# Optimization experiments

Hardware: AMD Instinct MI355X
Metric: run time of the kernel (lower is better)

## Reference

```python
import jax, jax.numpy as jnp
import numpy as np

B, N, S, K = 4, 32768, 8192, 16
IN_C, OUT_C = 64, 128
MID = max(OUT_C // 4, 8)  # attn_mlp hidden = 32
GN_GROUPS = 8
EPS = 1e-5


def setup_inputs() -> dict:
    key = jax.random.key(0)
    ks = jax.random.split(key, 16)
    def lin(k, out_c, in_c):
        # torch nn.Linear default init: U(-1/sqrt(in), 1/sqrt(in)), weight shape (out, in)
        bound = 1.0 / np.sqrt(in_c)
        return jax.random.uniform(k, (out_c, in_c), jnp.float32, -bound, bound)
    return {
        "xyz": jax.random.normal(ks[0], (B, N, 3), jnp.float32),
        "feats": jax.random.normal(ks[1], (B, N, IN_C), jnp.float32),
        "idx_fps": jax.random.randint(ks[2], (B, S), 0, N),
        "idx_knn": jax.random.randint(ks[3], (B, S, K), 0, N),
        "Wq": lin(ks[4], OUT_C, IN_C),
        "Wk": lin(ks[5], OUT_C, IN_C),
        "Wv": lin(ks[6], OUT_C, IN_C),
        "Wp1": lin(ks[7], OUT_C, 3),
        "Wp2": lin(ks[8], OUT_C, OUT_C),
        "Wa1": lin(ks[9], MID, OUT_C),
        "Wa2": lin(ks[10], OUT_C, MID),
        "Wproj": lin(ks[11], OUT_C, OUT_C),
        "ln_w": jnp.ones((OUT_C,), jnp.float32),
        "ln_b": jnp.zeros((OUT_C,), jnp.float32),
        "Wres": lin(ks[12], OUT_C, IN_C),
        "Wpost": lin(ks[13], OUT_C, OUT_C),
        "gn_w": jnp.ones((OUT_C,), jnp.float32),
        "gn_b": jnp.zeros((OUT_C,), jnp.float32),
    }


def _gather(x, idx):
    # x: (B, N, C); idx: (B, ...) -> (B, ..., C)
    return jax.vmap(lambda xb, ib: xb[ib])(x, idx)


def _layer_norm(x, w, b):
    mu = x.mean(-1, keepdims=True)
    var = x.var(-1, keepdims=True)
    return (x - mu) * jax.lax.rsqrt(var + EPS) * w + b


def _group_norm(x, w, b):
    # x: (B, S, C); normalize per (batch, group) over (S, C//G) — matches GroupNorm on (B,C,L)
    Bx, Sx, C = x.shape
    xg = x.reshape(Bx, Sx, GN_GROUPS, C // GN_GROUPS)
    mu = xg.mean(axis=(1, 3), keepdims=True)
    var = xg.var(axis=(1, 3), keepdims=True)
    xn = (xg - mu) * jax.lax.rsqrt(var + EPS)
    return xn.reshape(Bx, Sx, C) * w + b


def _forward(xyz, feats, idx_fps, idx_knn, Wq, Wk, Wv, Wp1, Wp2, Wa1, Wa2,
             Wproj, ln_w, ln_b, Wres, Wpost, gn_w, gn_b):
    s_xyz = _gather(xyz, idx_fps)        # (B,S,3)
    s_feat = _gather(feats, idx_fps)     # (B,S,C_in)
    n_xyz = _gather(xyz, idx_knn)        # (B,S,k,3)
    n_feat = _gather(feats, idx_knn)     # (B,S,k,C_in)

    # LocalAttentionBlock (Point Transformer v1 subtraction attention)
    q = jnp.einsum('bsc,oc->bso', s_feat, Wq)[:, :, None, :]   # (B,S,1,O)
    kk = jnp.einsum('bskc,oc->bsko', n_feat, Wk)               # (B,S,k,O)
    v = jnp.einsum('bskc,oc->bsko', n_feat, Wv)
    rel = n_xyz - s_xyz[:, :, None, :]                         # (B,S,k,3)
    pe = jnp.einsum('bskm,om->bsko',
                    jax.nn.relu(jnp.einsum('bskc,oc->bsko', rel, Wp1)), Wp2)
    h = q - kk + pe
    w = jnp.einsum('bskm,om->bsko',
                   jax.nn.relu(jnp.einsum('bsko,mo->bskm', h, Wa1)), Wa2)
    w = jax.nn.softmax(w, axis=2)                              # softmax over k
    out = jnp.sum(w * (v + pe), axis=2)                        # (B,S,O)
    out = jnp.einsum('bso,po->bsp', out, Wproj)
    res = jnp.einsum('bsc,oc->bso', s_feat, Wres)
    out = _layer_norm(out + res, ln_w, ln_b)

    # post: Conv1d(1x1, no bias) -> GroupNorm(8) -> ReLU
    out = jnp.einsum('bso,po->bsp', out, Wpost)
    out = jax.nn.relu(_group_norm(out, gn_w, gn_b))
    return s_xyz, out


def reference(xyz, feats, idx_fps, idx_knn, Wq, Wk, Wv, Wp1, Wp2, Wa1, Wa2,
              Wproj, ln_w, ln_b, Wres, Wpost, gn_w, gn_b):
    return _forward(xyz, feats, idx_fps, idx_knn, Wq, Wk, Wv, Wp1, Wp2, Wa1,
                    Wa2, Wproj, ln_w, ln_b, Wres, Wpost, gn_w, gn_b)
```

## Files before the change

kernel.cpp:

```cpp
#include <hip/hip_runtime.h>
#include <hip/hip_bf16.h>
#include <math.h>

#define B_ 4
#define N_ 32768
#define S_ 8192
#define K_ 16
#define CIN 64
#define COUT 128
#define MID_ 32
#define EPS_ 1e-5f
#define NTILE 2048

typedef __attribute__((ext_vector_type(8))) short s16x8;
typedef __attribute__((ext_vector_type(4))) float f32x4;

__device__ ushort g_attn[(size_t)B_ * S_ * COUT];
__device__ ushort g_sfeat[(size_t)B_ * S_ * CIN];
__device__ float  g_part[NTILE * 8 * 2];
__device__ float  g_stats[64];
__device__ float  g_fw[8192];

__device__ __forceinline__ uint pk2(float lo, float hi) {
  __hip_bfloat162 h = __float22bfloat162_rn(make_float2(lo, hi));
  return *(uint*)&h;
}
__device__ __forceinline__ ushort f2bf(float f) {
  __hip_bfloat16 h = __float2bfloat16(f);
  return *(ushort*)&h;
}
__device__ __forceinline__ int4 pack8(float4 a, float4 b) {
  int4 o;
  o.x = pk2(a.x, a.y); o.y = pk2(a.z, a.w);
  o.z = pk2(b.x, b.y); o.w = pk2(b.z, b.w);
  return o;
}
__device__ __forceinline__ f32x4 mfma16(s16x8 a, s16x8 b, f32x4 c) {
  return __builtin_amdgcn_mfma_f32_16x16x32_bf16(a, b, c, 0, 0, 0);
}
__device__ __forceinline__ int sw7(int row) { return (row & 7) ^ ((row & 8) >> 2); }
__device__ __forceinline__ int sw2(int row) { return (row & 3) ^ ((row >> 2) & 3); }

__device__ __forceinline__ s16x8 ldw256(const ushort* W, int row, int g) {
  return *(const s16x8*)((const char*)W + row * 256 + ((g ^ (row & 7)) << 4));
}
__device__ __forceinline__ s16x8 ldw128(const ushort* W, int row, int g) {
  return *(const s16x8*)((const char*)W + row * 128 + ((g ^ (row & 7)) << 4));
}
__device__ __forceinline__ s16x8 ldfrag_g8(const float* p) {
  float4 a = *(const float4*)p, b = *(const float4*)(p + 4);
  union { int4 i; s16x8 s; } u;
  u.i = pack8(a, b);
  return u.s;
}
__device__ __forceinline__ void st16h(char* bufb, int t, f32x4 c, int l, int cq,
                                      bool dorelu) {
  const int colp = (l & 15) + 16 * t;
  const int g = colp >> 3;
  const int off = (colp & 7) * 2;
  #pragma unroll
  for (int rr = 0; rr < 4; ++rr) {
    const int row = cq * 4 + rr;
    float v = dorelu ? fmaxf(c[rr], 0.f) : c[rr];
    *(ushort*)(bufb + row * 128 + ((g ^ sw7(row)) << 4) + off) = f2bf(v);
  }
}
__device__ __forceinline__ void st16_a1(char* bufb, int t, f32x4 c, int l, int cq) {
  const int colp = (l & 15) + 16 * t;
  const int g = colp >> 3;
  const int off = (colp & 7) * 2;
  #pragma unroll
  for (int rr = 0; rr < 4; ++rr) {
    const int row = cq * 4 + rr;
    *(ushort*)(bufb + row * 64 + ((g ^ sw2(row)) << 4) + off) =
        f2bf(fmaxf(c[rr], 0.f));
  }
}
__device__ __forceinline__ void st16p(char* bufb, int t, f32x4 c, int l, int cq) {
  const int colp = (l & 15) + 16 * t;
  const int g = colp >> 3;
  const int off = (colp & 7) * 2;
  #pragma unroll
  for (int rr = 0; rr < 4; ++rr) {
    const int row = cq * 4 + rr;
    *(ushort*)(bufb + row * 256 + ((g ^ (row & 15)) << 4) + off) = f2bf(c[rr]);
  }
}

__global__ __launch_bounds__(256) void k_fuse(
    const float* __restrict__ Wq, const float* __restrict__ Wk,
    const float* __restrict__ Wp2, const float* __restrict__ Wa1)
{
  const int t = blockIdx.x * 256 + threadIdx.x;
  if (t < 2048) {
    int m = t >> 6, c = t & 63;
    float s = 0.f;
    for (int o = 0; o < COUT; ++o) s += Wa1[m * COUT + o] * Wq[o * CIN + c];
    g_fw[t] = s;
  } else if (t < 4096) {
    int u = t - 2048;
    int m = u >> 6, c = u & 63;
    float s = 0.f;
    for (int o = 0; o < COUT; ++o) s += Wa1[m * COUT + o] * Wk[o * CIN + c];
    g_fw[t] = s;
  } else {
    int u = t - 4096;
    int m = u >> 7, c = u & 127;
    float s = 0.f;
    for (int o = 0; o < COUT; ++o) s += Wa1[m * COUT + o] * Wp2[o * COUT + c];
    g_fw[t] = s;
  }
}

__global__ __launch_bounds__(768) void k_attn(
    const float* __restrict__ xyz, const float* __restrict__ feats,
    const int* __restrict__ idx_fps, const int* __restrict__ idx_knn,
    const float* __restrict__ Wv, const float* __restrict__ Wp1,
    const float* __restrict__ Wp2, const float* __restrict__ Wa2,
    float* __restrict__ out_xyz)
{
  __shared__ ushort lWv[COUT * CIN];
  __shared__ ushort lWp1[COUT * 8];
  __shared__ ushort lWp2[COUT * COUT];
  __shared__ ushort lWka1[MID_ * CIN];
  __shared__ ushort lWpa1[MID_ * COUT];
  __shared__ ushort sbuf[12 * 1024];

  const int tid = threadIdx.x;
  const int w = tid >> 6, l = tid & 63;
  const int r = l & 15, cq = l >> 4;

  for (int i = tid; i < COUT * CIN / 2; i += 768) {
    int row = i >> 5; int kp = (i & 31) * 2;
    int g = kp >> 3;
    *(uint*)((char*)lWv + row * 128 + ((g ^ (row & 7)) << 4) + (kp & 7) * 2)
        = pk2(Wv[row * CIN + kp], Wv[row * CIN + kp + 1]);
  }
  if (tid < 512) {
    int row = tid >> 2; int kp = (tid & 3) * 2;
    float lo = (kp < 3) ? Wp1[row * 3 + kp] : 0.f;
    float hi = (kp + 1 < 3) ? Wp1[row * 3 + kp + 1] : 0.f;
    *(uint*)((char*)lWp1 + row * 16 + kp * 2) = pk2(lo, hi);
  }
  for (int i = tid; i < COUT * CIN; i += 768) {
    int row = i >> 6; int kp = (i & 63) * 2;
    int g = kp >> 3;
    *(uint*)((char*)lWp2 + row * 256 + ((g ^ (row & 7)) << 4) + (kp & 7) * 2)
        = pk2(Wp2[row * COUT + kp], Wp2[row * COUT + kp + 1]);
  }
  for (int i = tid; i < MID_ * CIN / 2; i += 768) {
    int row = i >> 5; int kp = (i & 31) * 2;
    int g = kp >> 3;
    const float* src = g_fw + 2048 + row * CIN + kp;
    *(uint*)((char*)lWka1 + row * 128 + ((g ^ (row & 7)) << 4) + (kp & 7) * 2)
        = pk2(-src[0], -src[1]);
  }
  for (int i = tid; i < MID_ * COUT / 2; i += 768) {
    int row = i >> 6; int kp = (i & 63) * 2;
    int g = kp >> 3;
    const float* src = g_fw + 4096 + row * COUT + kp;
    *(uint*)((char*)lWpa1 + row * 256 + ((g ^ (row & 7)) << 4) + (kp & 7) * 2)
        = pk2(src[0], src[1]);
  }

  s16x8 fWa2[8];
  #pragma unroll
  for (int t = 0; t < 8; ++t)
    fWa2[t] = ldfrag_g8(Wa2 + (16 * t + r) * MID_ + cq * 8);

  __syncthreads();

  char* bufb = (char*)(sbuf + w * 1024);
  const int cnt  = (w < 8) ? 11 : 10;
  const int pid0 = blockIdx.x * 128 + ((w < 8) ? w * 11 : 88 + (w - 8) * 10);

  {
    const int rp = (r < cnt) ? r : 0;
    const int p = pid0 + rp;
    const int bb = p >> 13;
    const int si = idx_fps[p];
    const float* fs = feats + ((size_t)bb * N_ + si) * CIN;
    #pragma unroll
    for (int j = 0; j < 2; ++j) {
      int g = cq * 2 + j;
      int4 pks = pack8(*(const float4*)(fs + g * 8), *(const float4*)(fs + g * 8 + 4));
      *(int4*)(bufb + r * 128 + ((g ^ sw7(r)) << 4)) = pks;
      if (r < cnt) *(int4*)((char*)g_sfeat + (size_t)p * 128 + g * 16) = pks;
    }
    if (l < 3 * cnt) {
      int pi = l / 3, j = l - pi * 3;
      int pp = pid0 + pi;
      out_xyz[(size_t)pp * 3 + j] =
          xyz[((size_t)(pp >> 13) * N_ + idx_fps[pp]) * 3 + j];
    }
  }
  f32x4 qa1[2];
  qa1[0] = (f32x4){0, 0, 0, 0}; qa1[1] = (f32x4){0, 0, 0, 0};
  {
    s16x8 fS[2], fQ;
    #pragma unroll
    for (int ks = 0; ks < 2; ++ks)
      fS[ks] = *(const s16x8*)(bufb + r * 128 + (((ks * 4 + cq) ^ sw7(r)) << 4));
    #pragma unroll
    for (int ks = 0; ks < 2; ++ks)
      #pragma unroll
      for (int t = 0; t < 2; ++t) {
        fQ = ldfrag_g8(g_fw + (16 * t + r) * CIN + ks * 32 + cq * 8);
        qa1[t] = mfma16(fS[ks], fQ, qa1[t]);
      }
  }

  #pragma unroll 1
  for (int i = 0; i < cnt; ++i) {
    const int pid = pid0 + i;
    const int bb = pid >> 13;
    const int nid = idx_knn[(size_t)pid * K_ + r];
    const float* fn = feats + ((size_t)bb * N_ + nid) * CIN + cq * 16;
    float4 f0 = ((const float4*)fn)[0], f1 = ((const float4*)fn)[1];
    float4 f2 = ((const float4*)fn)[2], f3 = ((const float4*)fn)[3];

    s16x8 fRel = {0, 0, 0, 0, 0, 0, 0, 0};
    if (cq == 0) {
      const float* xn = xyz + ((size_t)bb * N_ + nid) * 3;
      const float* xs = xyz + ((size_t)bb * N_ + idx_fps[pid]) * 3;
      fRel[0] = (short)f2bf(xn[0] - xs[0]);
      fRel[1] = (short)f2bf(xn[1] - xs[1]);
      fRel[2] = (short)f2bf(xn[2] - xs[2]);
    }

    {
      int g0 = cq * 2;
      *(int4*)(bufb + r * 128 + ((g0 ^ sw7(r)) << 4)) = pack8(f0, f1);
      *(int4*)(bufb + r * 128 + (((g0 + 1) ^ sw7(r)) << 4)) = pack8(f2, f3);
    }

    s16x8 fA[2];
    #pragma unroll
    for (int ks = 0; ks < 2; ++ks)
      fA[ks] = *(const s16x8*)(bufb + r * 128 + (((ks * 4 + cq) ^ sw7(r)) << 4));

    #pragma unroll
    for (int t = 0; t < 4; ++t) {
      f32x4 z = {0, 0, 0, 0};
      f32x4 c = mfma16(fRel, *(const s16x8*)((const char*)lWp1 + (16 * t + r) * 16), z);
      st16h(bufb, t, c, l, cq, true);
    }

    __builtin_amdgcn_s_setprio(1);
    f32x4 vv[8];
    #pragma unroll
    for (int t = 0; t < 8; ++t) vv[t] = (f32x4){0, 0, 0, 0};
    #pragma unroll
    for (int ks = 0; ks < 2; ++ks)
      #pragma unroll
      for (int t = 0; t < 8; ++t)
        vv[t] = mfma16(fA[ks], ldw128(lWv, 16 * t + r, ks * 4 + cq), vv[t]);
    f32x4 za[2];
    za[0] = (f32x4){0, 0, 0, 0}; za[1] = (f32x4){0, 0, 0, 0};
    #pragma unroll
    for (int ks = 0; ks < 2; ++ks)
      #pragma unroll
      for (int t = 0; t < 2; ++t)
        za[t] = mfma16(fA[ks], ldw128(lWka1, 16 * t + r, ks * 4 + cq), za[t]);
    __builtin_amdgcn_s_setprio(0);

    s16x8 fT0[2];
    #pragma unroll
    for (int ks = 0; ks < 2; ++ks)
      fT0[ks] = *(const s16x8*)(bufb + r * 128 + (((ks * 4 + cq) ^ sw7(r)) << 4));

    #pragma unroll
    for (int t = 0; t < 4; ++t) {
      f32x4 z = {0, 0, 0, 0};
      f32x4 c = mfma16(fRel,
                       *(const s16x8*)((const char*)lWp1 + (16 * (t + 4) + r) * 16), z);
      st16h(bufb, t, c, l, cq, true);
    }

    __builtin_amdgcn_s_setprio(1);
    #pragma unroll
    for (int ks = 0; ks < 2; ++ks)
      #pragma unroll
      for (int t = 0; t < 8; ++t)
        vv[t] = mfma16(fT0[ks], ldw256(lWp2, 16 * t + r, ks * 4 + cq), vv[t]);
    #pragma unroll
    for (int ks = 0; ks < 2; ++ks)
      #pragma unroll
      for (int t = 0; t < 2; ++t)
        za[t] = mfma16(fT0[ks], ldw256(lWpa1, 16 * t + r, ks * 4 + cq), za[t]);
    __builtin_amdgcn_s_setprio(0);

    s16x8 fT1[2];
    #pragma unroll
    for (int ks = 0; ks < 2; ++ks)
      fT1[ks] = *(const s16x8*)(bufb + r * 128 + (((ks * 4 + cq) ^ sw7(r)) << 4));

    __builtin_amdgcn_s_setprio(1);
    #pragma unroll
    for (int ks = 0; ks < 2; ++ks)
      #pragma unroll
      for (int t = 0; t < 8; ++t)
        vv[t] = mfma16(fT1[ks], ldw256(lWp2, 16 * t + r, (ks + 2) * 4 + cq), vv[t]);
    #pragma unroll
    for (int ks = 0; ks < 2; ++ks)
      #pragma unroll
      for (int t = 0; t < 2; ++t)
        za[t] = mfma16(fT1[ks], ldw256(lWpa1, 16 * t + r, (ks + 2) * 4 + cq), za[t]);
    __builtin_amdgcn_s_setprio(0);

    const int ii = i & 3, iq = i >> 2;
    #pragma unroll
    for (int t = 0; t < 2; ++t) {
      float qsel = ii == 0 ? qa1[t][0] : ii == 1 ? qa1[t][1]
                 : ii == 2 ? qa1[t][2] : qa1[t][3];
      float qv = __shfl(qsel, (iq << 4) + (l & 15));
      f32x4 ta = za[t];
      #pragma unroll
      for (int rr = 0; rr < 4; ++rr) ta[rr] += qv;
      st16_a1(bufb, t, ta, l, cq);
    }
    s16x8 fA1 = *(const s16x8*)(bufb + r * 64 + ((cq ^ sw2(r)) << 4));
    #pragma unroll
    for (int t = 0; t < 8; ++t) {
      f32x4 z = {0, 0, 0, 0};
      f32x4 wwt = mfma16(fA1, fWa2[t], z);
      float m = fmaxf(fmaxf(wwt[0], wwt[1]), fmaxf(wwt[2], wwt[3]));
      m = fmaxf(m, __shfl_xor(m, 16));
      m = fmaxf(m, __shfl_xor(m, 32));
      float e0 = __expf(wwt[0] - m), e1 = __expf(wwt[1] - m);
      float e2 = __expf(wwt[2] - m), e3 = __expf(wwt[3] - m);
      float ss = e0 + e1 + e2 + e3;
      ss += __shfl_xor(ss, 16);
      ss += __shfl_xor(ss, 32);
      float acc = e0 * vv[t][0] + e1 * vv[t][1] + e2 * vv[t][2] + e3 * vv[t][3];
      acc += __shfl_xor(acc, 16);
      acc += __shfl_xor(acc, 32);
      float outv = acc / ss;
      if (cq == (t >> 2)) {
        int colp = (l & 15) + 16 * t;
        *(ushort*)((char*)g_attn + (size_t)pid * 256 + colp * 2) = f2bf(outv);
      }
    }
  }
}

__global__ __launch_bounds__(512, 2) void k_post(
    const float* __restrict__ Wproj, const float* __restrict__ Wres,
    const float* __restrict__ Wpost, const float* __restrict__ ln_w,
    const float* __restrict__ ln_b, float* __restrict__ out_main)
{
  __shared__ ushort lWpj[COUT * COUT];
  __shared__ ushort lWrs[COUT * CIN];
  __shared__ ushort lWps[COUT * COUT];
  __shared__ float  llnw[COUT], llnb[COUT];
  __shared__ ushort sbuf[8 * 16 * COUT];

  const int tid = threadIdx.x;
  const int w = tid >> 6, l = tid & 63;
  const int r = l & 15, cq = l >> 4;

  for (int i = tid; i < COUT * CIN; i += 512) {
    int row = i >> 6; int kp = (i & 63) * 2;
    int g = kp >> 3;
    *(uint*)((char*)lWpj + row * 256 + ((g ^ (row & 7)) << 4) + (kp & 7) * 2)
        = pk2(Wproj[row * COUT + kp], Wproj[row * COUT + kp + 1]);
  }
  for (int i = tid; i < COUT * CIN / 2; i += 512) {
    int row = i >> 5; int kp = (i & 31) * 2;
    int g = kp >> 3;
    *(uint*)((char*)lWrs + row * 128 + ((g ^ (row & 7)) << 4) + (kp & 7) * 2)
        = pk2(Wres[row * CIN + kp], Wres[row * CIN + kp + 1]);
  }
  for (int i = tid; i < COUT * CIN; i += 512) {
    int row = i >> 6; int kp = (i & 63) * 2;
    int g = kp >> 3;
    *(uint*)((char*)lWps + row * 256 + ((g ^ (row & 7)) << 4) + (kp & 7) * 2)
        = pk2(Wpost[row * COUT + kp], Wpost[row * COUT + kp + 1]);
  }
  if (tid < COUT) { llnw[tid] = ln_w[tid]; llnb[tid] = ln_b[tid]; }
  __syncthreads();

  const int T = blockIdx.x * 8 + w;
  char* bufb = (char*)(sbuf + w * 16 * COUT);

  f32x4 acc[8];
  #pragma unroll
  for (int t = 0; t < 8; ++t) acc[t] = (f32x4){0, 0, 0, 0};

  s16x8 fA[4];
  #pragma unroll
  for (int ks = 0; ks < 4; ++ks)
    fA[ks] = *(const s16x8*)(g_attn + ((size_t)T * 16 + r) * COUT + ks * 32 + cq * 8);
  #pragma unroll
  for (int ks = 0; ks < 4; ++ks)
    #pragma unroll
    for (int t = 0; t < 8; ++t)
      acc[t] = mfma16(fA[ks], ldw256(lWpj, 16 * t + r, ks * 4 + cq), acc[t]);

  s16x8 fS[2];
  #pragma unroll
  for (int ks = 0; ks < 2; ++ks)
    fS[ks] = *(const s16x8*)(g_sfeat + ((size_t)T * 16 + r) * CIN + ks * 32 + cq * 8);
  #pragma unroll
  for (int ks = 0; ks < 2; ++ks)
    #pragma unroll
    for (int t = 0; t < 8; ++t)
      acc[t] = mfma16(fS[ks], ldw128(lWrs, 16 * t + r, ks * 4 + cq), acc[t]);

  #pragma unroll
  for (int rr = 0; rr < 4; ++rr) {
    float s1 = 0.f, s2 = 0.f;
    #pragma unroll
    for (int t = 0; t < 8; ++t) { float v = acc[t][rr]; s1 += v; s2 += v * v; }
    #pragma unroll
    for (int off = 1; off < 16; off <<= 1) {
      s1 += __shfl_xor(s1, off);
      s2 += __shfl_xor(s2, off);
    }
    float mu = s1 * (1.f / COUT);
    float rs = rsqrtf(s2 * (1.f / COUT) - mu * mu + EPS_);
    #pragma unroll
    for (int t = 0; t < 8; ++t) {
      int col = (l & 15) + 16 * t;
      acc[t][rr] = (acc[t][rr] - mu) * rs * llnw[col] + llnb[col];
    }
  }
  #pragma unroll
  for (int t = 0; t < 8; ++t) st16p(bufb, t, acc[t], l, cq);

  s16x8 fZ[4];
  #pragma unroll
  for (int ks = 0; ks < 4; ++ks)
    fZ[ks] = *(const s16x8*)(bufb + r * 256 + (((ks * 4 + cq) ^ (r & 15)) << 4));
  f32x4 po[8];
  #pragma unroll
  for (int t = 0; t < 8; ++t) po[t] = (f32x4){0, 0, 0, 0};
  #pragma unroll
  for (int ks = 0; ks < 4; ++ks)
    #pragma unroll
    for (int t = 0; t < 8; ++t)
      po[t] = mfma16(fZ[ks], ldw256(lWps, 16 * t + r, ks * 4 + cq), po[t]);

  #pragma unroll
  for (int t = 0; t < 8; ++t) {
    float s1 = po[t][0] + po[t][1] + po[t][2] + po[t][3];
    float s2 = po[t][0] * po[t][0] + po[t][1] * po[t][1]
             + po[t][2] * po[t][2] + po[t][3] * po[t][3];
    #pragma unroll
    for (int off = 1; off < 64; off <<= 1) {
      s1 += __shfl_xor(s1, off);
      s2 += __shfl_xor(s2, off);
    }
    if (l == 0) {
      g_part[((size_t)T * 8 + t) * 2] = s1;
      g_part[((size_t)T * 8 + t) * 2 + 1] = s2;
    }
    #pragma unroll
    for (int rr = 0; rr < 4; ++rr) {
      int row = T * 16 + cq * 4 + rr;
      out_main[(size_t)row * COUT + (l & 15) + 16 * t] = po[t][rr];
    }
  }
}

__global__ void k_gn_finish(void) {
  int bg = blockIdx.x;
  int b = bg >> 3, g = bg & 7;
  int t = threadIdx.x;
  float s1 = 0.f, s2 = 0.f;
  for (int i = t; i < 512; i += 64) {
    size_t T = (size_t)b * 512 + i;
    s1 += g_part[(T * 8 + g) * 2];
    s2 += g_part[(T * 8 + g) * 2 + 1];
  }
  #pragma unroll
  for (int off = 1; off < 64; off <<= 1) {
    s1 += __shfl_xor(s1, off);
    s2 += __shfl_xor(s2, off);
  }
  if (t == 0) {
    float n = (float)S_ * 16.f;
    float mu = s1 / n;
    float var = s2 / n - mu * mu;
    g_stats[bg * 2] = mu;
    g_stats[bg * 2 + 1] = rsqrtf(var + EPS_);
  }
}

__global__ __launch_bounds__(256) void k_gn_apply(
    float* __restrict__ x, const float* __restrict__ gn_w,
    const float* __restrict__ gn_b)
{
  const int i = blockIdx.x * 256 + threadIdx.x;
  if (i >= B_ * S_ * (COUT / 4)) return;
  const int c = (i & 31) * 4;
  const int g = c >> 4;
  const int b = i >> 18;
  const float m = g_stats[(b * 8 + g) * 2];
  const float rv = g_stats[(b * 8 + g) * 2 + 1];
  float4 v = ((float4*)x)[i];
  v.x = fmaxf((v.x - m) * rv * gn_w[c + 0] + gn_b[c + 0], 0.f);
  v.y = fmaxf((v.y - m) * rv * gn_w[c + 1] + gn_b[c + 1], 0.f);
  v.z = fmaxf((v.z - m) * rv * gn_w[c + 2] + gn_b[c + 2], 0.f);
  v.w = fmaxf((v.w - m) * rv * gn_w[c + 3] + gn_b[c + 3], 0.f);
  ((float4*)x)[i] = v;
}

extern "C" void kernel_launch(void* const* d_in, const int* in_sizes, int n_in,
                              void* d_out, int out_size, void* d_ws, size_t ws_size,
                              hipStream_t stream) {
  const float* xyz     = (const float*)d_in[0];
  const float* feats   = (const float*)d_in[1];
  const int*   idx_fps = (const int*)d_in[2];
  const int*   idx_knn = (const int*)d_in[3];
  const float* Wq    = (const float*)d_in[4];
  const float* Wk    = (const float*)d_in[5];
  const float* Wv    = (const float*)d_in[6];
  const float* Wp1   = (const float*)d_in[7];
  const float* Wp2   = (const float*)d_in[8];
  const float* Wa1   = (const float*)d_in[9];
  const float* Wa2   = (const float*)d_in[10];
  const float* Wproj = (const float*)d_in[11];
  const float* ln_w  = (const float*)d_in[12];
  const float* ln_b  = (const float*)d_in[13];
  const float* Wres  = (const float*)d_in[14];
  const float* Wpost = (const float*)d_in[15];
  const float* gn_w  = (const float*)d_in[16];
  const float* gn_b  = (const float*)d_in[17];

  float* out      = (float*)d_out;
  float* out_xyz  = out;
  float* out_main = out + (size_t)B_ * S_ * 3;

  k_fuse<<<dim3(32), dim3(256), 0, stream>>>(Wq, Wk, Wp2, Wa1);
  k_attn<<<dim3(256), dim3(768), 0, stream>>>(
      xyz, feats, idx_fps, idx_knn, Wv, Wp1, Wp2, Wa2, out_xyz);
  k_post<<<dim3(256), dim3(512), 0, stream>>>(
      Wproj, Wres, Wpost, ln_w, ln_b, out_main);
  k_gn_finish<<<dim3(32), dim3(64), 0, stream>>>();
  k_gn_apply<<<dim3((B_ * S_ * (COUT / 4) + 255) / 256), dim3(256), 0, stream>>>(
      out_main, gn_w, gn_b);
}
```

Measured before the change: 122.1 us.

## Compute V per output tile inside softmax loop to cut registers, raise occupancy

The 32-register vv accumulator array is dropped. Each 16-column V+PE tile is now computed on demand inside the softmax/aggregation loop, which lowers register pressure. With that, the attention kernel moves from 256 blocks of 768 threads to 512 blocks of 512 threads, with launch_bounds(512,2) so two blocks fit per CU. Each wave now handles 8 points, and the setprio hints are removed. The risk is that the fT0/fT1/fA fragments stay live longer, and the MFMA chains inside the softmax loop are serialized, with less independent work between them.

```diff
diff --git a/kernel.cpp b/kernel.cpp
--- a/kernel.cpp
+++ b/kernel.cpp
@@ -112,7 +112,7 @@
   }
 }
 
-__global__ __launch_bounds__(768) void k_attn(
+__global__ __launch_bounds__(512, 2) void k_attn(
     const float* __restrict__ xyz, const float* __restrict__ feats,
     const int* __restrict__ idx_fps, const int* __restrict__ idx_knn,
     const float* __restrict__ Wv, const float* __restrict__ Wp1,
@@ -124,38 +124,38 @@
   __shared__ ushort lWp2[COUT * COUT];
   __shared__ ushort lWka1[MID_ * CIN];
   __shared__ ushort lWpa1[MID_ * COUT];
-  __shared__ ushort sbuf[12 * 1024];
+  __shared__ ushort sbuf[8 * 1024];
 
   const int tid = threadIdx.x;
   const int w = tid >> 6, l = tid & 63;
   const int r = l & 15, cq = l >> 4;
 
-  for (int i = tid; i < COUT * CIN / 2; i += 768) {
+  for (int i = tid; i < COUT * CIN / 2; i += 512) {
     int row = i >> 5; int kp = (i & 31) * 2;
     int g = kp >> 3;
     *(uint*)((char*)lWv + row * 128 + ((g ^ (row & 7)) << 4) + (kp & 7) * 2)
         = pk2(Wv[row * CIN + kp], Wv[row * CIN + kp + 1]);
   }
-  if (tid < 512) {
+  {
     int row = tid >> 2; int kp = (tid & 3) * 2;
     float lo = (kp < 3) ? Wp1[row * 3 + kp] : 0.f;
     float hi = (kp + 1 < 3) ? Wp1[row * 3 + kp + 1] : 0.f;
     *(uint*)((char*)lWp1 + row * 16 + kp * 2) = pk2(lo, hi);
   }
-  for (int i = tid; i < COUT * CIN; i += 768) {
+  for (int i = tid; i < COUT * CIN; i += 512) {
     int row = i >> 6; int kp = (i & 63) * 2;
     int g = kp >> 3;
     *(uint*)((char*)lWp2 + row * 256 + ((g ^ (row & 7)) << 4) + (kp & 7) * 2)
         = pk2(Wp2[row * COUT + kp], Wp2[row * COUT + kp + 1]);
   }
-  for (int i = tid; i < MID_ * CIN / 2; i += 768) {
+  for (int i = tid; i < MID_ * CIN / 2; i += 512) {
     int row = i >> 5; int kp = (i & 31) * 2;
     int g = kp >> 3;
     const float* src = g_fw + 2048 + row * CIN + kp;
     *(uint*)((char*)lWka1 + row * 128 + ((g ^ (row & 7)) << 4) + (kp & 7) * 2)
         = pk2(-src[0], -src[1]);
   }
-  for (int i = tid; i < MID_ * COUT / 2; i += 768) {
+  for (int i = tid; i < MID_ * COUT / 2; i += 512) {
     int row = i >> 6; int kp = (i & 63) * 2;
     int g = kp >> 3;
     const float* src = g_fw + 4096 + row * COUT + kp;
@@ -171,12 +171,10 @@
   __syncthreads();
 
   char* bufb = (char*)(sbuf + w * 1024);
-  const int cnt  = (w < 8) ? 11 : 10;
-  const int pid0 = blockIdx.x * 128 + ((w < 8) ? w * 11 : 88 + (w - 8) * 10);
+  const int pid0 = (blockIdx.x * 8 + w) * 8;
 
   {
-    const int rp = (r < cnt) ? r : 0;
-    const int p = pid0 + rp;
+    const int p = pid0 + (r & 7);
     const int bb = p >> 13;
     const int si = idx_fps[p];
     const float* fs = feats + ((size_t)bb * N_ + si) * CIN;
@@ -185,9 +183,9 @@
       int g = cq * 2 + j;
       int4 pks = pack8(*(const float4*)(fs + g * 8), *(const float4*)(fs + g * 8 + 4));
       *(int4*)(bufb + r * 128 + ((g ^ sw7(r)) << 4)) = pks;
-      if (r < cnt) *(int4*)((char*)g_sfeat + (size_t)p * 128 + g * 16) = pks;
-    }
-    if (l < 3 * cnt) {
+      if (r < 8) *(int4*)((char*)g_sfeat + (size_t)p * 128 + g * 16) = pks;
+    }
+    if (l < 24) {
       int pi = l / 3, j = l - pi * 3;
       int pp = pid0 + pi;
       out_xyz[(size_t)pp * 3 + j] =
@@ -211,7 +209,7 @@
   }
 
   #pragma unroll 1
-  for (int i = 0; i < cnt; ++i) {
+  for (int i = 0; i < 8; ++i) {
     const int pid = pid0 + i;
     const int bb = pid >> 13;
     const int nid = idx_knn[(size_t)pid * K_ + r];
@@ -246,15 +244,6 @@
       st16h(bufb, t, c, l, cq, true);
     }
 
-    __builtin_amdgcn_s_setprio(1);
-    f32x4 vv[8];
-    #pragma unroll
-    for (int t = 0; t < 8; ++t) vv[t] = (f32x4){0, 0, 0, 0};
-    #pragma unroll
-    for (int ks = 0; ks < 2; ++ks)
-      #pragma unroll
-      for (int t = 0; t < 8; ++t)
-        vv[t] = mfma16(fA[ks], ldw128(lWv, 16 * t + r, ks * 4 + cq), vv[t]);
     f32x4 za[2];
     za[0] = (f32x4){0, 0, 0, 0}; za[1] = (f32x4){0, 0, 0, 0};
     #pragma unroll
@@ -262,7 +251,6 @@
       #pragma unroll
       for (int t = 0; t < 2; ++t)
         za[t] = mfma16(fA[ks], ldw128(lWka1, 16 * t + r, ks * 4 + cq), za[t]);
-    __builtin_amdgcn_s_setprio(0);
 
     s16x8 fT0[2];
     #pragma unroll
@@ -277,36 +265,22 @@
       st16h(bufb, t, c, l, cq, true);
     }
 
-    __builtin_amdgcn_s_setprio(1);
-    #pragma unroll
-    for (int ks = 0; ks < 2; ++ks)
-      #pragma unroll
-      for (int t = 0; t < 8; ++t)
-        vv[t] = mfma16(fT0[ks], ldw256(lWp2, 16 * t + r, ks * 4 + cq), vv[t]);
     #pragma unroll
     for (int ks = 0; ks < 2; ++ks)
       #pragma unroll
       for (int t = 0; t < 2; ++t)
         za[t] = mfma16(fT0[ks], ldw256(lWpa1, 16 * t + r, ks * 4 + cq), za[t]);
-    __builtin_amdgcn_s_setprio(0);
 
     s16x8 fT1[2];
     #pragma unroll
     for (int ks = 0; ks < 2; ++ks)
       fT1[ks] = *(const s16x8*)(bufb + r * 128 + (((ks * 4 + cq) ^ sw7(r)) << 4));
 
-    __builtin_amdgcn_s_setprio(1);
-    #pragma unroll
-    for (int ks = 0; ks < 2; ++ks)
-      #pragma unroll
-      for (int t = 0; t < 8; ++t)
-        vv[t] = mfma16(fT1[ks], ldw256(lWp2, 16 * t + r, (ks + 2) * 4 + cq), vv[t]);
     #pragma unroll
     for (int ks = 0; ks < 2; ++ks)
       #pragma unroll
       for (int t = 0; t < 2; ++t)
         za[t] = mfma16(fT1[ks], ldw256(lWpa1, 16 * t + r, (ks + 2) * 4 + cq), za[t]);
-    __builtin_amdgcn_s_setprio(0);
 
     const int ii = i & 3, iq = i >> 2;
     #pragma unroll
@@ -320,8 +294,19 @@
       st16_a1(bufb, t, ta, l, cq);
     }
     s16x8 fA1 = *(const s16x8*)(bufb + r * 64 + ((cq ^ sw2(r)) << 4));
+
     #pragma unroll
     for (int t = 0; t < 8; ++t) {
+      f32x4 vt = {0, 0, 0, 0};
+      #pragma unroll
+      for (int ks = 0; ks < 2; ++ks)
+        vt = mfma16(fA[ks], ldw128(lWv, 16 * t + r, ks * 4 + cq), vt);
+      #pragma unroll
+      for (int ks = 0; ks < 2; ++ks)
+        vt = mfma16(fT0[ks], ldw256(lWp2, 16 * t + r, ks * 4 + cq), vt);
+      #pragma unroll
+      for (int ks = 0; ks < 2; ++ks)
+        vt = mfma16(fT1[ks], ldw256(lWp2, 16 * t + r, (ks + 2) * 4 + cq), vt);
       f32x4 z = {0, 0, 0, 0};
       f32x4 wwt = mfma16(fA1, fWa2[t], z);
       float m = fmaxf(fmaxf(wwt[0], wwt[1]), fmaxf(wwt[2], wwt[3]));
@@ -332,7 +317,7 @@
       float ss = e0 + e1 + e2 + e3;
       ss += __shfl_xor(ss, 16);
       ss += __shfl_xor(ss, 32);
-      float acc = e0 * vv[t][0] + e1 * vv[t][1] + e2 * vv[t][2] + e3 * vv[t][3];
+      float acc = e0 * vt[0] + e1 * vt[1] + e2 * vt[2] + e3 * vt[3];
       acc += __shfl_xor(acc, 16);
       acc += __shfl_xor(acc, 32);
       float outv = acc / ss;
@@ -533,7 +518,7 @@
   float* out_main = out + (size_t)B_ * S_ * 3;
 
   k_fuse<<<dim3(32), dim3(256), 0, stream>>>(Wq, Wk, Wp2, Wa1);
-  k_attn<<<dim3(256), dim3(768), 0, stream>>>(
+  k_attn<<<dim3(512), dim3(512), 0, stream>>>(
       xyz, feats, idx_fps, idx_knn, Wv, Wp1, Wp2, Wa2, out_xyz);
   k_post<<<dim3(256), dim3(512), 0, stream>>>(
       Wproj, Wres, Wpost, ln_w, ln_b, out_main);
```

After: 144.4 us. 1.18x slower.
